# Kernel optimization log

Measured on AMD Instinct MI355X. Metric: run time of the kernel, lower is better.

The kernel has to match this reference:

```python
import jax, jax.numpy as jnp
import numpy as np

HIDDEN = 1280
HEADS = 8
RANK = 4
BATCH = 2
SEQ = 4096


def setup_inputs() -> dict:
    key = jax.random.key(0)
    ks = jax.random.split(key, 11)
    s = 1.0 / np.sqrt(HIDDEN)
    return {
        "hidden_states": jax.random.normal(ks[0], (BATCH, SEQ, HIDDEN), jnp.float32),
        # attn projections (stored as [in, out] for x @ W)
        "w_q": jax.random.normal(ks[1], (HIDDEN, HIDDEN), jnp.float32) * s,
        "w_k": jax.random.normal(ks[2], (HIDDEN, HIDDEN), jnp.float32) * s,
        "w_v": jax.random.normal(ks[3], (HIDDEN, HIDDEN), jnp.float32) * s,
        # LoRA down/up matrices for K and V
        "lora_k_a": jax.random.normal(ks[4], (HIDDEN, RANK), jnp.float32) * s,
        "lora_k_b": jax.random.normal(ks[5], (RANK, HIDDEN), jnp.float32) * 0.5,
        "lora_v_a": jax.random.normal(ks[6], (HIDDEN, RANK), jnp.float32) * s,
        "lora_v_b": jax.random.normal(ks[7], (RANK, HIDDEN), jnp.float32) * 0.5,
        # output projection (to_out[0]); to_out[1] is dropout -> identity at eval
        "w_out": jax.random.normal(ks[8], (HIDDEN, HIDDEN), jnp.float32) * s,
        "b_out": jax.random.normal(ks[9], (HIDDEN,), jnp.float32) * 0.01,
    }


def reference(hidden_states, w_q, w_k, w_v, lora_k_a, lora_k_b,
              lora_v_a, lora_v_b, w_out, b_out):
    B, S, D = hidden_states.shape
    H = HEADS
    dh = D // H
    scale = 1.0 / np.sqrt(dh)

    # QKV projections
    q = hidden_states @ w_q                      # [B, S, D]
    k = hidden_states @ w_k
    v = hidden_states @ w_v

    # LoRA low-rank residual updates to key/value
    k = k + (k @ lora_k_a) @ lora_k_b            # rank-4 update
    v = v + (v @ lora_v_a) @ lora_v_b

    # head_to_batch_dim: [B, S, D] -> [B, H, S, dh]
    q = q.reshape(B, S, H, dh).transpose(0, 2, 1, 3)
    k = k.reshape(B, S, H, dh).transpose(0, 2, 1, 3)
    v = v.reshape(B, S, H, dh).transpose(0, 2, 1, 3)

    # naive attention: scores -> softmax -> weighted sum
    scores = jnp.einsum("bhqd,bhkd->bhqk", q, k) * scale   # [B, H, S, S]
    probs = jax.nn.softmax(scores, axis=-1)
    out = jnp.einsum("bhqk,bhkd->bhqd", probs, v)          # [B, H, S, dh]

    # batch_to_head_dim: [B, H, S, dh] -> [B, S, D]
    out = out.transpose(0, 2, 1, 3).reshape(B, S, D)

    # to_out[0] linear; to_out[1] dropout is identity in eval
    return out @ w_out + b_out
```

## Files before the change

### kernel.cpp

```cpp
#include <hip/hip_runtime.h>
#include <stdint.h>

typedef __attribute__((ext_vector_type(8))) __bf16 bf16x8;
typedef __attribute__((ext_vector_type(2))) __bf16 bf16x2;
typedef __attribute__((ext_vector_type(4))) float f32x4;
typedef __attribute__((ext_vector_type(16))) float f32x16;
typedef unsigned short u16;

#define LOG2E 1.44269504088896f

static_assert(sizeof(bf16x8) == 16, "bf16x8 must be 16B");

__device__ __forceinline__ u16 f2bf(float f) {
  unsigned u = __builtin_bit_cast(unsigned, f);
  u += 0x7fffu + ((u >> 16) & 1u);
  return (u16)(u >> 16);
}

__device__ __forceinline__ void load_lds16(const void* g, void* l) {
  __builtin_amdgcn_global_load_lds((const __attribute__((address_space(1))) void*)g,
                                   (__attribute__((address_space(3))) void*)l, 16, 0, 0);
}

__global__ __launch_bounds__(256) void lora_tmp_k(
    const float* __restrict__ wk, const float* __restrict__ wv,
    const float* __restrict__ ka, const float* __restrict__ va,
    float* __restrict__ tk, float* __restrict__ tv) {
  const int i = blockIdx.x;
  const float* W = blockIdx.y ? wv : wk;
  const float* A = blockIdx.y ? va : ka;
  float* T = blockIdx.y ? tv : tk;
  float s0 = 0.f, s1 = 0.f, s2 = 0.f, s3 = 0.f;
  for (int j = threadIdx.x; j < 1280; j += 256) {
    float w = W[(size_t)i * 1280 + j];
    float4 a4 = *(const float4*)(A + (size_t)j * 4);
    s0 += w * a4.x; s1 += w * a4.y; s2 += w * a4.z; s3 += w * a4.w;
  }
#pragma unroll
  for (int m = 1; m < 64; m <<= 1) {
    s0 += __shfl_xor(s0, m); s1 += __shfl_xor(s1, m);
    s2 += __shfl_xor(s2, m); s3 += __shfl_xor(s3, m);
  }
  __shared__ float red[4][4];
  const int wv_ = threadIdx.x >> 6;
  if ((threadIdx.x & 63) == 0) {
    red[wv_][0] = s0; red[wv_][1] = s1; red[wv_][2] = s2; red[wv_][3] = s3;
  }
  __syncthreads();
  if (threadIdx.x < 4) {
    float r = red[0][threadIdx.x] + red[1][threadIdx.x] + red[2][threadIdx.x] + red[3][threadIdx.x];
    T[(size_t)i * 4 + threadIdx.x] = r;
  }
}

__global__ void wt_prep_k(const float* __restrict__ wq, const float* __restrict__ wk,
                          const float* __restrict__ wv, const float* __restrict__ wo,
                          const float* __restrict__ tk, const float* __restrict__ tv,
                          const float* __restrict__ lkb, const float* __restrict__ lvb,
                          u16* __restrict__ WTbase) {
  const int z = blockIdx.z;
  const float* W = (z == 0) ? wq : (z == 1) ? wk : (z == 2) ? wv : wo;
  const float* tmp = (z == 1) ? tk : (z == 2) ? tv : nullptr;
  const float* LB = (z == 1) ? lkb : (z == 2) ? lvb : nullptr;
  u16* WT = WTbase + (size_t)z * 1638400;
  __shared__ float tile[32][33];
  const int o0 = blockIdx.x * 32, i0 = blockIdx.y * 32;
  const int tx = threadIdx.x, ty = threadIdx.y;
#pragma unroll
  for (int kk = 0; kk < 4; ++kk) {
    int i = i0 + ty + kk * 8, o = o0 + tx;
    float v = W[(size_t)i * 1280 + o];
    if (tmp) {
      float4 t = *(const float4*)(tmp + (size_t)i * 4);
      v += t.x * LB[o] + t.y * LB[1280 + o] + t.z * LB[2560 + o] + t.w * LB[3840 + o];
    }
    tile[ty + kk * 8][tx] = v;
  }
  __syncthreads();
#pragma unroll
  for (int kk = 0; kk < 4; ++kk) {
    int o = o0 + ty + kk * 8, i = i0 + tx;
    WT[(size_t)o * 1280 + i] = f2bf(tile[tx][ty + kk * 8]);
  }
}

__global__ __launch_bounds__(256) void cvt_bf16_k(const float* __restrict__ in,
                                                  u16* __restrict__ out, int n4) {
  for (int i = blockIdx.x * 256 + threadIdx.x; i < n4; i += gridDim.x * 256) {
    float4 v = ((const float4*)in)[i];
    ushort4 o;
    o.x = f2bf(v.x); o.y = f2bf(v.y); o.z = f2bf(v.z); o.w = f2bf(v.w);
    ((ushort4*)out)[i] = o;
  }
}

__global__ void vtrans_k(const u16* __restrict__ V, u16* __restrict__ VT) {
  __shared__ u16 tile[32][33];
  const int s0 = blockIdx.x * 32, c0 = blockIdx.y * 32, b = blockIdx.z;
  const int tx = threadIdx.x, ty = threadIdx.y;
#pragma unroll
  for (int kk = 0; kk < 4; ++kk)
    tile[ty + kk * 8][tx] = V[(size_t)(b * 4096 + s0 + ty + kk * 8) * 1280 + c0 + tx];
  __syncthreads();
#pragma unroll
  for (int kk = 0; kk < 4; ++kk)
    VT[(size_t)(b * 1280 + c0 + ty + kk * 8) * 4096 + s0 + tx] = tile[tx][ty + kk * 8];
}

template <bool F32OUT, bool FUSED3>
__global__ __launch_bounds__(256) void gemm128_k(
    const u16* __restrict__ A, const u16* __restrict__ WT,
    void* __restrict__ outp, const float* __restrict__ bias, float oscale) {
  __shared__ __align__(16) u16 lds[2 * 128 * 40];
  u16* ldsA = lds;
  u16* ldsB = lds + 128 * 40;
  const int tid = threadIdx.x;
  const int lane = tid & 63, lrow = lane & 15, lhi = lane >> 4;
  const int w = tid >> 6, wm = w >> 1, wn = w & 1;
  const size_t M0 = (size_t)blockIdx.x * 128, N0 = (size_t)blockIdx.y * 128;
  const int wb = tid & 192;
  f32x4 acc[4][4] = {};

  for (int k0 = 0; k0 < 1280; k0 += 32) {
#pragma unroll
    for (int j = 0; j < 3; ++j) {
      if (j < 2 || tid < 128) {
        int i = j * 256 + tid;
        int row = i / 5, c = i % 5; c = c < 4 ? c : 3;
        load_lds16(A + (M0 + row) * 1280 + k0 + c * 8, ldsA + (j * 256 + wb) * 8);
      }
    }
#pragma unroll
    for (int j = 0; j < 3; ++j) {
      if (j < 2 || tid < 128) {
        int i = j * 256 + tid;
        int row = i / 5, c = i % 5; c = c < 4 ? c : 3;
        load_lds16(WT + (N0 + row) * 1280 + k0 + c * 8, ldsB + (j * 256 + wb) * 8);
      }
    }
    __syncthreads();
    bf16x8 af[4], bfr[4];
#pragma unroll
    for (int m = 0; m < 4; ++m)
      af[m] = *(const bf16x8*)(ldsA + (wm * 64 + m * 16 + lrow) * 40 + lhi * 8);
#pragma unroll
    for (int n = 0; n < 4; ++n)
      bfr[n] = *(const bf16x8*)(ldsB + (wn * 64 + n * 16 + lrow) * 40 + lhi * 8);
#pragma unroll
    for (int m = 0; m < 4; ++m)
#pragma unroll
      for (int n = 0; n < 4; ++n)
        acc[m][n] = __builtin_amdgcn_mfma_f32_16x16x32_bf16(af[m], bfr[n], acc[m][n], 0, 0, 0);
    __syncthreads();
  }

  const float sc = FUSED3 ? (N0 < 1280 ? oscale : 1.0f) : oscale;
  const size_t obase = FUSED3 ? (size_t)(N0 / 1280) * 10485760 : 0;
  const size_t ncol0 = FUSED3 ? (N0 % 1280) : N0;
#pragma unroll
  for (int m = 0; m < 4; ++m)
#pragma unroll
    for (int n = 0; n < 4; ++n)
#pragma unroll
      for (int r = 0; r < 4; ++r) {
        size_t row = M0 + wm * 64 + m * 16 + lhi * 4 + r;
        size_t col = ncol0 + wn * 64 + n * 16 + lrow;
        float v = acc[m][n][r];
        if (F32OUT)
          ((float*)outp)[row * 1280 + col] = v + bias[col];
        else
          ((u16*)outp)[obase + row * 1280 + col] = f2bf(v * sc);
      }
}


#define QK_CLUSTER(KCUR)                                                        \
  {                                                                             \
    f32x16 zz = {};                                                             \
    sacc0 = zz; sacc1 = zz;                                                     \
    __builtin_amdgcn_s_setprio(1);                                              \
    _Pragma("unroll")                                                           \
    for (int kf = 0; kf < 10; ++kf) {                                           \
      const int c_ = 2 * kf + lhi5;                                             \
      {                                                                         \
        const int row_ = l31;                                                   \
        const int slot_ = (kf < 8) ? ((c_ & 24) | ((c_ ^ row_) & 7))            \
                                   : (16 + ((c_ ^ (row_ >> 1)) & 3));           \
        bf16x8 ka_ = *(const bf16x8*)((KCUR) + row_ * 160 + slot_ * 8);         \
        sacc0 = __builtin_amdgcn_mfma_f32_32x32x16_bf16(ka_, qf[kf], sacc0, 0, 0, 0); \
      }                                                                         \
      {                                                                         \
        const int row_ = 32 + l31;                                              \
        const int slot_ = (kf < 8) ? ((c_ & 24) | ((c_ ^ row_) & 7))            \
                                   : (16 + ((c_ ^ (row_ >> 1)) & 3));           \
        bf16x8 ka_ = *(const bf16x8*)((KCUR) + row_ * 160 + slot_ * 8);         \
        sacc1 = __builtin_amdgcn_mfma_f32_32x32x16_bf16(ka_, qf[kf], sacc1, 0, 0, 0); \
      }                                                                         \
    }                                                                           \
    __builtin_amdgcn_s_setprio(0);                                              \
  }

#define PV_CLUSTER(VSRC)                                                        \
  {                                                                             \
    __builtin_amdgcn_s_setprio(1);                                              \
    _Pragma("unroll")                                                           \
    for (int kf = 0; kf < 4; ++kf) {                                            \
      const int base_ = (kf >> 1) * 8 + (kf & 1) * 4;                           \
      unsigned xa_ = xp[base_ + 0], xb_ = xp[base_ + 1];                        \
      unsigned xc_ = xp[base_ + 2], xd_ = xp[base_ + 3];                        \
      unsigned sa_ = __shfl_xor((int)xa_, 32), sb_ = __shfl_xor((int)xb_, 32);  \
      unsigned sc_ = __shfl_xor((int)xc_, 32), sd_ = __shfl_xor((int)xd_, 32);  \
      uint4 pw_;                                                                \
      pw_.x = lo32 ? xa_ : sc_;                                                 \
      pw_.y = lo32 ? xb_ : sd_;                                                 \
      pw_.z = lo32 ? sa_ : xc_;                                                 \
      pw_.w = lo32 ? sb_ : xd_;                                                 \
      bf16x8 pB_ = __builtin_bit_cast(bf16x8, pw_);                             \
      const int c_ = 2 * kf + lhi5;                                             \
      _Pragma("unroll")                                                         \
      for (int dm = 0; dm < 5; ++dm) {                                          \
        const int row_ = dm * 32 + l31;                                         \
        bf16x8 va_ = *(const bf16x8*)((VSRC) + row_ * 64 + ((c_ ^ (row_ & 7)) * 8)); \
        o[dm] = __builtin_amdgcn_mfma_f32_32x32x16_bf16(va_, pB_, o[dm], 0, 0, 0); \
      }                                                                         \
    }                                                                           \
    __builtin_amdgcn_s_setprio(0);                                              \
  }

#define SOFTMAX_STEP()                                                          \
  {                                                                             \
    float tmx_[8];                                                              \
    _Pragma("unroll")                                                           \
    for (int i = 0; i < 8; ++i)                                                 \
      tmx_[i] = fmaxf(fmaxf(sacc0[i], sacc0[i + 8]),                            \
                      fmaxf(sacc1[i], sacc1[i + 8]));                           \
    float mx_ = fmaxf(fmaxf(fmaxf(tmx_[0], tmx_[1]), fmaxf(tmx_[2], tmx_[3])),  \
                      fmaxf(fmaxf(tmx_[4], tmx_[5]), fmaxf(tmx_[6], tmx_[7]))); \
    mx_ = fmaxf(mx_, __shfl_xor(mx_, 32));                                      \
    if (__any(mx_ - m_run > 8.0f)) {                                            \
      float mnew_ = fmaxf(m_run, mx_);                                          \
      float al_ = __builtin_amdgcn_exp2f((m_run - mnew_) * LOG2E);              \
      l_run *= al_; m_run = mnew_; mLog = m_run * LOG2E;                        \
      _Pragma("unroll")                                                         \
      for (int dm = 0; dm < 5; ++dm)                                            \
        _Pragma("unroll")                                                       \
        for (int i = 0; i < 16; ++i) o[dm][i] *= al_;                           \
    }                                                                           \
    float rs0_ = 0.f, rs1_ = 0.f, rs2_ = 0.f, rs3_ = 0.f;                       \
    _Pragma("unroll")                                                           \
    for (int r = 0; r < 8; ++r) {                                               \
      float p0_ = __builtin_amdgcn_exp2f(fmaf(sacc0[2 * r], LOG2E, -mLog));     \
      float p1_ = __builtin_amdgcn_exp2f(fmaf(sacc0[2 * r + 1], LOG2E, -mLog)); \
      if ((r & 3) == 0) rs0_ += p0_ + p1_;                                      \
      else if ((r & 3) == 1) rs1_ += p0_ + p1_;                                 \
      else if ((r & 3) == 2) rs2_ += p0_ + p1_;                                 \
      else rs3_ += p0_ + p1_;                                                   \
      bf16x2 pk_; pk_[0] = (__bf16)p0_; pk_[1] = (__bf16)p1_;                   \
      xp[r] = __builtin_bit_cast(unsigned, pk_);                                \
    }                                                                           \
    _Pragma("unroll")                                                           \
    for (int r = 0; r < 8; ++r) {                                               \
      float p0_ = __builtin_amdgcn_exp2f(fmaf(sacc1[2 * r], LOG2E, -mLog));     \
      float p1_ = __builtin_amdgcn_exp2f(fmaf(sacc1[2 * r + 1], LOG2E, -mLog)); \
      if ((r & 3) == 0) rs0_ += p0_ + p1_;                                      \
      else if ((r & 3) == 1) rs1_ += p0_ + p1_;                                 \
      else if ((r & 3) == 2) rs2_ += p0_ + p1_;                                 \
      else rs3_ += p0_ + p1_;                                                   \
      bf16x2 pk_; pk_[0] = (__bf16)p0_; pk_[1] = (__bf16)p1_;                   \
      xp[8 + r] = __builtin_bit_cast(unsigned, pk_);                            \
    }                                                                           \
    float rs_ = (rs0_ + rs1_) + (rs2_ + rs3_);                                  \
    rs_ += __shfl_xor(rs_, 32);                                                 \
    l_run += rs_;                                                               \
  }

#define STAGE_K(KV0, DST)                                                       \
  {                                                                             \
    _Pragma("unroll")                                                           \
    for (int j = 0; j < 5; ++j) {                                               \
      int i_ = j * 256 + tid;                                                   \
      int row_ = i_ / 20, cl_ = i_ % 20;                                        \
      int cg_ = (cl_ < 16) ? ((cl_ & 24) | ((cl_ ^ row_) & 7))                  \
                           : (16 + ((cl_ ^ (row_ >> 1)) & 3));                  \
      load_lds16(Kg + (size_t)((KV0) + row_) * 1280 + cg_ * 8,                  \
                 (DST) + (j * 256 + wb) * 8);                                   \
    }                                                                           \
  }

#define STAGE_V(KV0, DST)                                                       \
  {                                                                             \
    _Pragma("unroll")                                                           \
    for (int j = 0; j < 5; ++j) {                                               \
      int i_ = j * 256 + tid;                                                   \
      int row_ = i_ >> 3, cl_ = i_ & 7;                                         \
      int cg_ = cl_ ^ (row_ & 7);                                               \
      load_lds16(VTg + (size_t)row_ * 4096 + (KV0) + cg_ * 8,                   \
                 (DST) + (j * 256 + wb) * 8);                                   \
    }                                                                           \
  }

#define WAITB(N)                                                                \
  asm volatile("s_waitcnt vmcnt(" #N ")" ::: "memory");                         \
  __builtin_amdgcn_s_barrier();                                                 \
  __builtin_amdgcn_sched_barrier(0);

__global__ __launch_bounds__(256, 2) void attn_k(
    const u16* __restrict__ Q, const u16* __restrict__ K,
    const u16* __restrict__ VT, u16* __restrict__ AO) {
  __shared__ __align__(16) u16 lds_all[40960];
  u16* const kb0 = lds_all;
  u16* const kb1 = lds_all + 10240;
  u16* const vt0 = lds_all + 20480;
  u16* const vt1 = lds_all + 30720;
  const int tid = threadIdx.x;
  const int lane = tid & 63;
  const int l31 = lane & 31, lhi5 = lane >> 5;
  const int lo32 = (lane < 32);
  const int w = tid >> 6;
  const int nid = ((blockIdx.x & 7) << 6) | (blockIdx.x >> 3);
  const int bh = nid >> 5, qt = nid & 31;
  const int b = bh >> 3, h = bh & 7;
  const int wb = tid & 192;

  const u16* Kg = K + (size_t)b * 4096 * 1280 + h * 160;
  const u16* VTg = VT + ((size_t)b * 1280 + h * 160) * 4096;

  bf16x8 qf[10];
  const u16* Qg = Q + (size_t)(b * 4096 + qt * 128 + w * 32 + l31) * 1280 + h * 160 + lhi5 * 8;
#pragma unroll
  for (int kf = 0; kf < 10; ++kf) qf[kf] = *(const bf16x8*)(Qg + kf * 16);
#pragma unroll
  for (int kf = 0; kf < 10; ++kf) asm volatile("" : "+v"(qf[kf]));

  f32x16 o[5] = {};
  f32x16 sacc0, sacc1;
  unsigned xp[16];
  float m_run = -1e30f, l_run = 0.f;
  float mLog = m_run * LOG2E;

  STAGE_K(0, kb0);
  WAITB(0);
  STAGE_K(64, kb1);
  STAGE_V(0, vt0);
  QK_CLUSTER(kb0);
  SOFTMAX_STEP();

  for (int tp = 0; tp < 31; ++tp) {
    const int t1 = 2 * tp + 1;
    WAITB(5);
    STAGE_K((t1 + 1) * 64, kb0);
    STAGE_V(t1 * 64, vt1);
    QK_CLUSTER(kb1);
    WAITB(10);
    PV_CLUSTER(vt0);
    SOFTMAX_STEP();
    WAITB(5);
    STAGE_K((t1 + 2) * 64, kb1);
    STAGE_V((t1 + 1) * 64, vt0);
    QK_CLUSTER(kb0);
    WAITB(10);
    PV_CLUSTER(vt1);
    SOFTMAX_STEP();
  }

  WAITB(5);
  STAGE_V(63 * 64, vt1);
  QK_CLUSTER(kb1);
  WAITB(5);
  PV_CLUSTER(vt0);
  SOFTMAX_STEP();

  WAITB(0);
  PV_CLUSTER(vt1);

  float invl = 1.f / l_run;
  u16* tr = lds_all + w * 5376;
#pragma unroll
  for (int dm = 0; dm < 5; ++dm)
#pragma unroll
    for (int k = 0; k < 4; ++k) {
      int d = dm * 32 + k * 8 + lhi5 * 4;
      unsigned lo_ = (unsigned)f2bf(o[dm][4 * k + 0] * invl) |
                     ((unsigned)f2bf(o[dm][4 * k + 1] * invl) << 16);
      unsigned hi_ = (unsigned)f2bf(o[dm][4 * k + 2] * invl) |
                     ((unsigned)f2bf(o[dm][4 * k + 3] * invl) << 16);
      uint2 u; u.x = lo_; u.y = hi_;
      *(uint2*)(tr + l31 * 168 + d) = u;
    }
  asm volatile("s_waitcnt lgkmcnt(0)" ::: "memory");
  __builtin_amdgcn_sched_barrier(0);
  const size_t qg0 = (size_t)(b * 4096 + qt * 128 + w * 32);
#pragma unroll
  for (int it = 0; it < 10; ++it) {
    int idx = it * 64 + lane;
    int row = idx / 20, cc = idx % 20;
    bf16x8 vch = *(const bf16x8*)(tr + row * 168 + cc * 8);
    *(bf16x8*)(AO + (qg0 + row) * 1280 + h * 160 + cc * 8) = vch;
  }
}

extern "C" void kernel_launch(void* const* d_in, const int* in_sizes, int n_in,
                              void* d_out, int out_size, void* d_ws, size_t ws_size,
                              hipStream_t stream) {
  const float* hs  = (const float*)d_in[0];
  const float* w_q = (const float*)d_in[1];
  const float* w_k = (const float*)d_in[2];
  const float* w_v = (const float*)d_in[3];
  const float* lka = (const float*)d_in[4];
  const float* lkb = (const float*)d_in[5];
  const float* lva = (const float*)d_in[6];
  const float* lvb = (const float*)d_in[7];
  const float* w_o = (const float*)d_in[8];
  const float* b_o = (const float*)d_in[9];
  float* out = (float*)d_out;
  char* ws = (char*)d_ws;

  const size_t KA  = 0;
  const size_t VA  = 20480;
  const size_t WTQ = 40960;
  const size_t WTO = WTQ + 3 * 3276800;
  const size_t HSB = WTO + 3276800;
  const size_t QB  = HSB + 20971520;
  const size_t KB  = QB + 20971520;
  const size_t VB  = KB + 20971520;
  const size_t VTB = VB + 20971520;
  const size_t AOB = VTB + 20971520;
  const size_t END = AOB + 20971520;
  if (ws_size < END) return;

  float* tk = (float*)(ws + KA);
  float* tv = (float*)(ws + VA);
  u16* wtq = (u16*)(ws + WTQ);
  u16* wto = (u16*)(ws + WTO);
  u16* hsb = (u16*)(ws + HSB);
  u16* qb  = (u16*)(ws + QB);
  u16* kb  = (u16*)(ws + KB);
  u16* vb  = (u16*)(ws + VB);
  u16* vtb = (u16*)(ws + VTB);
  u16* aob = (u16*)(ws + AOB);

  lora_tmp_k<<<dim3(1280, 2), 256, 0, stream>>>(w_k, w_v, lka, lva, tk, tv);
  wt_prep_k<<<dim3(40, 40, 4), dim3(32, 8), 0, stream>>>(w_q, w_k, w_v, w_o,
                                                         tk, tv, lkb, lvb, wtq);
  cvt_bf16_k<<<2048, 256, 0, stream>>>(hs, hsb, 2621440);

  const float qscale = 0.07905694150420949f;
  gemm128_k<false, true><<<dim3(64, 30), 256, 0, stream>>>(hsb, wtq, qb, nullptr, qscale);
  vtrans_k<<<dim3(128, 40, 2), dim3(32, 8), 0, stream>>>(vb, vtb);
  attn_k<<<dim3(512), 256, 0, stream>>>(qb, kb, vtb, aob);
  gemm128_k<true, false><<<dim3(64, 10), 256, 0, stream>>>(aob, wto, (void*)out, b_o, 1.0f);
}
```

Baseline: 375.9 us.

## Split attention KV range in halves with merge kernel and smaller tiles

The attention kernel now splits each query tile's key range into two halves handled by separate blocks (1024 blocks instead of 512), writing partial outputs plus per-row max/sum. A new merge kernel then combines the two halves with the log-sum-exp weights. K tiles shrink to 32 rows, V is single-buffered, and LDS use drops so three blocks can fit per CU. The aim is more parallelism and occupancy for the attention stage. The cost is an extra merge pass, extra memory traffic for the partial outputs, and an extra bf16 rounding of those partials.

```diff
diff --git a/kernel.cpp b/kernel.cpp
--- a/kernel.cpp
+++ b/kernel.cpp
@@ -15,6 +15,11 @@
   unsigned u = __builtin_bit_cast(unsigned, f);
   u += 0x7fffu + ((u >> 16) & 1u);
   return (u16)(u >> 16);
+}
+
+__device__ __forceinline__ float bf2f(u16 b) {
+  unsigned u = ((unsigned)b) << 16;
+  return __builtin_bit_cast(float, u);
 }
 
 __device__ __forceinline__ void load_lds16(const void* g, void* l) {
@@ -177,35 +182,25 @@
 #define QK_CLUSTER(KCUR)                                                        \
   {                                                                             \
     f32x16 zz = {};                                                             \
-    sacc0 = zz; sacc1 = zz;                                                     \
+    sacc0 = zz;                                                                 \
     __builtin_amdgcn_s_setprio(1);                                              \
     _Pragma("unroll")                                                           \
     for (int kf = 0; kf < 10; ++kf) {                                           \
       const int c_ = 2 * kf + lhi5;                                             \
-      {                                                                         \
-        const int row_ = l31;                                                   \
-        const int slot_ = (kf < 8) ? ((c_ & 24) | ((c_ ^ row_) & 7))            \
-                                   : (16 + ((c_ ^ (row_ >> 1)) & 3));           \
-        bf16x8 ka_ = *(const bf16x8*)((KCUR) + row_ * 160 + slot_ * 8);         \
-        sacc0 = __builtin_amdgcn_mfma_f32_32x32x16_bf16(ka_, qf[kf], sacc0, 0, 0, 0); \
-      }                                                                         \
-      {                                                                         \
-        const int row_ = 32 + l31;                                              \
-        const int slot_ = (kf < 8) ? ((c_ & 24) | ((c_ ^ row_) & 7))            \
-                                   : (16 + ((c_ ^ (row_ >> 1)) & 3));           \
-        bf16x8 ka_ = *(const bf16x8*)((KCUR) + row_ * 160 + slot_ * 8);         \
-        sacc1 = __builtin_amdgcn_mfma_f32_32x32x16_bf16(ka_, qf[kf], sacc1, 0, 0, 0); \
-      }                                                                         \
+      const int slot_ = (c_ < 16) ? ((c_ & 24) | ((c_ ^ l31) & 7))              \
+                                  : (16 + (((c_ - 16) ^ (l31 & 7)) & 7));       \
+      bf16x8 ka_ = *(const bf16x8*)((KCUR) + l31 * 192 + slot_ * 8);            \
+      sacc0 = __builtin_amdgcn_mfma_f32_32x32x16_bf16(ka_, qf[kf], sacc0, 0, 0, 0); \
     }                                                                           \
     __builtin_amdgcn_s_setprio(0);                                              \
   }
 
-#define PV_CLUSTER(VSRC)                                                        \
+#define PV_CLUSTER(SS)                                                          \
   {                                                                             \
     __builtin_amdgcn_s_setprio(1);                                              \
     _Pragma("unroll")                                                           \
-    for (int kf = 0; kf < 4; ++kf) {                                            \
-      const int base_ = (kf >> 1) * 8 + (kf & 1) * 4;                           \
+    for (int kf = 0; kf < 2; ++kf) {                                            \
+      const int base_ = kf * 4;                                                 \
       unsigned xa_ = xp[base_ + 0], xb_ = xp[base_ + 1];                        \
       unsigned xc_ = xp[base_ + 2], xd_ = xp[base_ + 3];                        \
       unsigned sa_ = __shfl_xor((int)xa_, 32), sb_ = __shfl_xor((int)xb_, 32);  \
@@ -216,11 +211,11 @@
       pw_.z = lo32 ? sa_ : xc_;                                                 \
       pw_.w = lo32 ? sb_ : xd_;                                                 \
       bf16x8 pB_ = __builtin_bit_cast(bf16x8, pw_);                             \
-      const int c_ = 2 * kf + lhi5;                                             \
+      const int c_ = (SS) * 4 + 2 * kf + lhi5;                                  \
       _Pragma("unroll")                                                         \
       for (int dm = 0; dm < 5; ++dm) {                                          \
         const int row_ = dm * 32 + l31;                                         \
-        bf16x8 va_ = *(const bf16x8*)((VSRC) + row_ * 64 + ((c_ ^ (row_ & 7)) * 8)); \
+        bf16x8 va_ = *(const bf16x8*)(vt + row_ * 64 + ((c_ ^ (row_ & 7)) * 8)); \
         o[dm] = __builtin_amdgcn_mfma_f32_32x32x16_bf16(va_, pB_, o[dm], 0, 0, 0); \
       }                                                                         \
     }                                                                           \
@@ -231,9 +226,7 @@
   {                                                                             \
     float tmx_[8];                                                              \
     _Pragma("unroll")                                                           \
-    for (int i = 0; i < 8; ++i)                                                 \
-      tmx_[i] = fmaxf(fmaxf(sacc0[i], sacc0[i + 8]),                            \
-                      fmaxf(sacc1[i], sacc1[i + 8]));                           \
+    for (int i = 0; i < 8; ++i) tmx_[i] = fmaxf(sacc0[i], sacc0[i + 8]);        \
     float mx_ = fmaxf(fmaxf(fmaxf(tmx_[0], tmx_[1]), fmaxf(tmx_[2], tmx_[3])),  \
                       fmaxf(fmaxf(tmx_[4], tmx_[5]), fmaxf(tmx_[6], tmx_[7]))); \
     mx_ = fmaxf(mx_, __shfl_xor(mx_, 32));                                      \
@@ -258,44 +251,34 @@
       bf16x2 pk_; pk_[0] = (__bf16)p0_; pk_[1] = (__bf16)p1_;                   \
       xp[r] = __builtin_bit_cast(unsigned, pk_);                                \
     }                                                                           \
-    _Pragma("unroll")                                                           \
-    for (int r = 0; r < 8; ++r) {                                               \
-      float p0_ = __builtin_amdgcn_exp2f(fmaf(sacc1[2 * r], LOG2E, -mLog));     \
-      float p1_ = __builtin_amdgcn_exp2f(fmaf(sacc1[2 * r + 1], LOG2E, -mLog)); \
-      if ((r & 3) == 0) rs0_ += p0_ + p1_;                                      \
-      else if ((r & 3) == 1) rs1_ += p0_ + p1_;                                 \
-      else if ((r & 3) == 2) rs2_ += p0_ + p1_;                                 \
-      else rs3_ += p0_ + p1_;                                                   \
-      bf16x2 pk_; pk_[0] = (__bf16)p0_; pk_[1] = (__bf16)p1_;                   \
-      xp[8 + r] = __builtin_bit_cast(unsigned, pk_);                            \
-    }                                                                           \
     float rs_ = (rs0_ + rs1_) + (rs2_ + rs3_);                                  \
     rs_ += __shfl_xor(rs_, 32);                                                 \
     l_run += rs_;                                                               \
   }
 
-#define STAGE_K(KV0, DST)                                                       \
+#define STAGE_K(T, DST)                                                         \
   {                                                                             \
     _Pragma("unroll")                                                           \
-    for (int j = 0; j < 5; ++j) {                                               \
+    for (int j = 0; j < 3; ++j) {                                               \
       int i_ = j * 256 + tid;                                                   \
-      int row_ = i_ / 20, cl_ = i_ % 20;                                        \
-      int cg_ = (cl_ < 16) ? ((cl_ & 24) | ((cl_ ^ row_) & 7))                  \
-                           : (16 + ((cl_ ^ (row_ >> 1)) & 3));                  \
-      load_lds16(Kg + (size_t)((KV0) + row_) * 1280 + cg_ * 8,                  \
+      int row_ = i_ / 24, cl_ = i_ % 24;                                        \
+      int cg_;                                                                  \
+      if (cl_ < 16) cg_ = (cl_ & 24) | ((cl_ ^ row_) & 7);                      \
+      else { int v_ = (cl_ - 16) ^ (row_ & 7); cg_ = (v_ < 4) ? 16 + v_ : 19; } \
+      load_lds16(Kg + (size_t)((T) * 32 + row_) * 1280 + cg_ * 8,               \
                  (DST) + (j * 256 + wb) * 8);                                   \
     }                                                                           \
   }
 
-#define STAGE_V(KV0, DST)                                                       \
+#define STAGE_V(P)                                                              \
   {                                                                             \
     _Pragma("unroll")                                                           \
     for (int j = 0; j < 5; ++j) {                                               \
       int i_ = j * 256 + tid;                                                   \
       int row_ = i_ >> 3, cl_ = i_ & 7;                                         \
       int cg_ = cl_ ^ (row_ & 7);                                               \
-      load_lds16(VTg + (size_t)row_ * 4096 + (KV0) + cg_ * 8,                   \
-                 (DST) + (j * 256 + wb) * 8);                                   \
+      load_lds16(VTg + (size_t)row_ * 4096 + (P) * 64 + cg_ * 8,                \
+                 vt + (j * 256 + wb) * 8);                                      \
     }                                                                           \
   }
 
@@ -304,26 +287,27 @@
   __builtin_amdgcn_s_barrier();                                                 \
   __builtin_amdgcn_sched_barrier(0);
 
-__global__ __launch_bounds__(256, 2) void attn_k(
+__global__ __launch_bounds__(256, 3) void attn_k(
     const u16* __restrict__ Q, const u16* __restrict__ K,
-    const u16* __restrict__ VT, u16* __restrict__ AO) {
-  __shared__ __align__(16) u16 lds_all[40960];
+    const u16* __restrict__ VT, u16* __restrict__ Y0g, u16* __restrict__ Y1g,
+    float2* __restrict__ ML) {
+  __shared__ __align__(16) u16 lds_all[22528];
   u16* const kb0 = lds_all;
-  u16* const kb1 = lds_all + 10240;
-  u16* const vt0 = lds_all + 20480;
-  u16* const vt1 = lds_all + 30720;
+  u16* const kb1 = lds_all + 6144;
+  u16* const vt = lds_all + 12288;
   const int tid = threadIdx.x;
   const int lane = tid & 63;
   const int l31 = lane & 31, lhi5 = lane >> 5;
   const int lo32 = (lane < 32);
   const int w = tid >> 6;
-  const int nid = ((blockIdx.x & 7) << 6) | (blockIdx.x >> 3);
-  const int bh = nid >> 5, qt = nid & 31;
+  const int nid = ((blockIdx.x & 7) << 7) | (blockIdx.x >> 3);
+  const int bh = nid >> 6, rem = nid & 63;
+  const int half = rem >> 5, qt = rem & 31;
   const int b = bh >> 3, h = bh & 7;
   const int wb = tid & 192;
 
-  const u16* Kg = K + (size_t)b * 4096 * 1280 + h * 160;
-  const u16* VTg = VT + ((size_t)b * 1280 + h * 160) * 4096;
+  const u16* Kg = K + (size_t)(b * 4096 + half * 2048) * 1280 + h * 160;
+  const u16* VTg = VT + ((size_t)b * 1280 + h * 160) * 4096 + half * 2048;
 
   bf16x8 qf[10];
   const u16* Qg = Q + (size_t)(b * 4096 + qt * 128 + w * 32 + l31) * 1280 + h * 160 + lhi5 * 8;
@@ -333,45 +317,45 @@
   for (int kf = 0; kf < 10; ++kf) asm volatile("" : "+v"(qf[kf]));
 
   f32x16 o[5] = {};
-  f32x16 sacc0, sacc1;
-  unsigned xp[16];
+  f32x16 sacc0;
+  unsigned xp[8];
   float m_run = -1e30f, l_run = 0.f;
   float mLog = m_run * LOG2E;
 
   STAGE_K(0, kb0);
   WAITB(0);
-  STAGE_K(64, kb1);
-  STAGE_V(0, vt0);
+  STAGE_V(0);
+  STAGE_K(1, kb1);
   QK_CLUSTER(kb0);
   SOFTMAX_STEP();
-
-  for (int tp = 0; tp < 31; ++tp) {
-    const int t1 = 2 * tp + 1;
+  WAITB(3);
+  PV_CLUSTER(0);
+
+  WAITB(0);
+  STAGE_K(2, kb0);
+  QK_CLUSTER(kb1);
+  SOFTMAX_STEP();
+  PV_CLUSTER(1);
+  __builtin_amdgcn_s_barrier();
+  __builtin_amdgcn_sched_barrier(0);
+  STAGE_V(1);
+
+  for (int p = 1; p < 32; ++p) {
     WAITB(5);
-    STAGE_K((t1 + 1) * 64, kb0);
-    STAGE_V(t1 * 64, vt1);
+    STAGE_K(2 * p + 1, kb1);
+    QK_CLUSTER(kb0);
+    SOFTMAX_STEP();
+    WAITB(3);
+    PV_CLUSTER(0);
+    WAITB(0);
+    if (p < 31) STAGE_K(2 * p + 2, kb0);
     QK_CLUSTER(kb1);
-    WAITB(10);
-    PV_CLUSTER(vt0);
     SOFTMAX_STEP();
-    WAITB(5);
-    STAGE_K((t1 + 2) * 64, kb1);
-    STAGE_V((t1 + 1) * 64, vt0);
-    QK_CLUSTER(kb0);
-    WAITB(10);
-    PV_CLUSTER(vt1);
-    SOFTMAX_STEP();
-  }
-
-  WAITB(5);
-  STAGE_V(63 * 64, vt1);
-  QK_CLUSTER(kb1);
-  WAITB(5);
-  PV_CLUSTER(vt0);
-  SOFTMAX_STEP();
-
-  WAITB(0);
-  PV_CLUSTER(vt1);
+    PV_CLUSTER(1);
+    __builtin_amdgcn_s_barrier();
+    __builtin_amdgcn_sched_barrier(0);
+    if (p < 31) STAGE_V(p + 1);
+  }
 
   float invl = 1.f / l_run;
   u16* tr = lds_all + w * 5376;
@@ -389,13 +373,52 @@
     }
   asm volatile("s_waitcnt lgkmcnt(0)" ::: "memory");
   __builtin_amdgcn_sched_barrier(0);
+  u16* Yw = half ? Y1g : Y0g;
   const size_t qg0 = (size_t)(b * 4096 + qt * 128 + w * 32);
 #pragma unroll
   for (int it = 0; it < 10; ++it) {
     int idx = it * 64 + lane;
     int row = idx / 20, cc = idx % 20;
     bf16x8 vch = *(const bf16x8*)(tr + row * 168 + cc * 8);
-    *(bf16x8*)(AO + (qg0 + row) * 1280 + h * 160 + cc * 8) = vch;
+    *(bf16x8*)(Yw + (qg0 + row) * 1280 + h * 160 + cc * 8) = vch;
+  }
+  if (lo32) {
+    float2 ml; ml.x = m_run; ml.y = l_run;
+    ML[((size_t)(half * 16 + bh)) * 4096 + qt * 128 + w * 32 + l31] = ml;
+  }
+}
+
+__global__ __launch_bounds__(256) void merge_k(
+    const u16* __restrict__ Y0, const u16* __restrict__ Y1,
+    const float2* __restrict__ ML, u16* __restrict__ OUT) {
+  const int total = 8192 * 160;
+  for (int c = blockIdx.x * 256 + threadIdx.x; c < total; c += gridDim.x * 256) {
+    int row = c / 160, dc = c % 160;
+    int h = dc / 20;
+    int b = row >> 12, q = row & 4095;
+    size_t mlbase = (size_t)(b * 8 + h) * 4096 + q;
+    float2 ml0 = ML[mlbase];
+    float2 ml1 = ML[(size_t)16 * 4096 + mlbase];
+    float m = fmaxf(ml0.x, ml1.x);
+    float a0 = ml0.y * __builtin_amdgcn_exp2f((ml0.x - m) * LOG2E);
+    float a1 = ml1.y * __builtin_amdgcn_exp2f((ml1.x - m) * LOG2E);
+    float inv = 1.f / (a0 + a1);
+    float w0 = a0 * inv, w1 = a1 * inv;
+    uint4 ya = ((const uint4*)Y0)[c];
+    uint4 yb = ((const uint4*)Y1)[c];
+    uint4 yo;
+    unsigned* pa = (unsigned*)&ya;
+    unsigned* pb = (unsigned*)&yb;
+    unsigned* po = (unsigned*)&yo;
+#pragma unroll
+    for (int k = 0; k < 4; ++k) {
+      float a_lo = bf2f((u16)(pa[k] & 0xffff)), a_hi = bf2f((u16)(pa[k] >> 16));
+      float b_lo = bf2f((u16)(pb[k] & 0xffff)), b_hi = bf2f((u16)(pb[k] >> 16));
+      unsigned lo = f2bf(a_lo * w0 + b_lo * w1);
+      unsigned hi = f2bf(a_hi * w0 + b_hi * w1);
+      po[k] = lo | (hi << 16);
+    }
+    ((uint4*)OUT)[c] = yo;
   }
 }
 
@@ -438,6 +461,8 @@
   u16* vb  = (u16*)(ws + VB);
   u16* vtb = (u16*)(ws + VTB);
   u16* aob = (u16*)(ws + AOB);
+  float2* ml = (float2*)hsb;
+  u16* merged = vtb;
 
   lora_tmp_k<<<dim3(1280, 2), 256, 0, stream>>>(w_k, w_v, lka, lva, tk, tv);
   wt_prep_k<<<dim3(40, 40, 4), dim3(32, 8), 0, stream>>>(w_q, w_k, w_v, w_o,
@@ -447,6 +472,7 @@
   const float qscale = 0.07905694150420949f;
   gemm128_k<false, true><<<dim3(64, 30), 256, 0, stream>>>(hsb, wtq, qb, nullptr, qscale);
   vtrans_k<<<dim3(128, 40, 2), dim3(32, 8), 0, stream>>>(vb, vtb);
-  attn_k<<<dim3(512), 256, 0, stream>>>(qb, kb, vtb, aob);
-  gemm128_k<true, false><<<dim3(64, 10), 256, 0, stream>>>(aob, wto, (void*)out, b_o, 1.0f);
-}
+  attn_k<<<dim3(1024), 256, 0, stream>>>(qb, kb, vtb, aob, vb, ml);
+  merge_k<<<dim3(5120), 256, 0, stream>>>(aob, vb, ml, merged);
+  gemm128_k<true, false><<<dim3(64, 10), 256, 0, stream>>>(merged, wto, (void*)out, b_o, 1.0f);
+}
```

Result: slower. 522.3 us (+38.9%).
